# Optimization experiments

Hardware: AMD Instinct MI355X
Metric: run time of the kernel (lower is better)

The kernel has to match this reference:

```python
import jax, jax.numpy as jnp
import numpy as np

B, T, D_IN, P, Q, D_OUT = 128, 1024, 64, 128, 2, 64


def _lstm_layer(x, w_ih, w_hh, b):
    """One LSTM layer, batch_first. x: [B,T,Din], w_ih: [4P,Din], w_hh: [4P,P], b: [4P].
    PyTorch gate order: i, f, g, o."""
    # Precompute input contribution for all timesteps (the big, parallel GEMM).
    gx = jnp.einsum('btd,gd->btg', x, w_ih) + b          # [B,T,4P]
    gx_t = jnp.swapaxes(gx, 0, 1)                        # [T,B,4P] for scan
    p = w_hh.shape[1]
    h0 = jnp.zeros((x.shape[0], p), dtype=x.dtype)
    c0 = jnp.zeros((x.shape[0], p), dtype=x.dtype)

    def step(carry, g_in):
        h, c = carry
        g = g_in + h @ w_hh.T                            # [B,4P]
        i, f, gg, o = jnp.split(g, 4, axis=-1)
        i = jax.nn.sigmoid(i)
        f = jax.nn.sigmoid(f)
        gg = jnp.tanh(gg)
        o = jax.nn.sigmoid(o)
        c = f * c + i * gg
        h = o * jnp.tanh(c)
        return (h, c), h

    _, hs = jax.lax.scan(step, (h0, c0), gx_t)           # hs: [T,B,P]
    return jnp.swapaxes(hs, 0, 1)                        # [B,T,P]


def setup_inputs() -> dict:
    key = jax.random.key(0)
    ks = jax.random.split(key, 8)
    x = jax.random.normal(ks[0], (B, T, D_IN), dtype=jnp.float32)
    # weight_ih: kaiming-normal-ish; weight_hh: orthogonal-ish (random normal is a fine stand-in
    # numerically; init distribution doesn't change the math being tested).
    w_ih0 = jax.random.normal(ks[1], (4 * P, D_IN), dtype=jnp.float32) * (1.0 / np.sqrt(D_IN))
    w_hh0 = jax.random.normal(ks[2], (4 * P, P), dtype=jnp.float32) * (1.0 / np.sqrt(P))
    w_ih1 = jax.random.normal(ks[3], (4 * P, P), dtype=jnp.float32) * (1.0 / np.sqrt(P))
    w_hh1 = jax.random.normal(ks[4], (4 * P, P), dtype=jnp.float32) * (1.0 / np.sqrt(P))
    # biases initialized to zero in the original (bias_ih + bias_hh folded into one per layer
    # would be equivalent math; keep both for faithfulness)
    b_ih = jnp.zeros((Q, 4 * P), dtype=jnp.float32)
    b_hh = jnp.zeros((Q, 4 * P), dtype=jnp.float32)
    fc_w = jax.random.normal(ks[5], (D_OUT, P), dtype=jnp.float32) * np.sqrt(2.0 / P)
    fc_b = jnp.zeros((D_OUT,), dtype=jnp.float32)
    return {"x": x, "w_ih0": w_ih0, "w_hh0": w_hh0, "w_ih1": w_ih1, "w_hh1": w_hh1,
            "b_ih": b_ih, "b_hh": b_hh, "fc_w": fc_w, "fc_b": fc_b}


def reference(x, w_ih0, w_hh0, w_ih1, w_hh1, b_ih, b_hh, fc_w, fc_b):
    h = _lstm_layer(x, w_ih0, w_hh0, b_ih[0] + b_hh[0])   # layer 0: [B,T,P]
    h = _lstm_layer(h, w_ih1, w_hh1, b_ih[1] + b_hh[1])   # layer 1: [B,T,P]
    return jnp.einsum('btp,op->bto', h, fc_w) + fc_b      # [B,T,D_OUT]
```

## Files before the change

### kernel.cpp

```cpp
#include <hip/hip_runtime.h>

#define NT 1024
#define RINGS 256

typedef _Float16 half8 __attribute__((ext_vector_type(8)));
typedef _Float16 half4 __attribute__((ext_vector_type(4)));
typedef float f32x4 __attribute__((ext_vector_type(4)));
typedef unsigned long long u64;
struct U2 { u64 a, b; };

__device__ __forceinline__ f32x4 MFMA(half8 a, half8 b, f32x4 c) {
  return __builtin_amdgcn_mfma_f32_16x16x32_f16(a, b, c, 0, 0, 0);
}
__device__ __forceinline__ float sigf(float x) {
  return __builtin_amdgcn_rcpf(1.0f + __expf(-x));
}
__device__ __forceinline__ float tanhf2(float x) {
  float ax = fabsf(x);
  float e = __expf(-2.0f * ax);
  float t = (1.0f - e) * __builtin_amdgcn_rcpf(1.0f + e);
  return copysignf(t, x);
}
__device__ __forceinline__ half8 cvt8(float4 c0, float4 c1) {
  half8 hv;
  hv[0] = (_Float16)c0.x; hv[1] = (_Float16)c0.y;
  hv[2] = (_Float16)c0.z; hv[3] = (_Float16)c0.w;
  hv[4] = (_Float16)c1.x; hv[5] = (_Float16)c1.y;
  hv[6] = (_Float16)c1.z; hv[7] = (_Float16)c1.w;
  return hv;
}
__device__ __forceinline__ half8 ldring(const _Float16* p) {
  const u64* q = (const u64*)p;
  U2 uu;
  uu.a = __hip_atomic_load(q, __ATOMIC_RELAXED, __HIP_MEMORY_SCOPE_AGENT);
  uu.b = __hip_atomic_load(q + 1, __ATOMIC_RELAXED, __HIP_MEMORY_SCOPE_AGENT);
  return __builtin_bit_cast(half8, uu);
}
__device__ __forceinline__ unsigned wpoll(unsigned* p, unsigned tgt,
                                          unsigned cached, int l) {
  unsigned c = cached;
  while (c < tgt) {
    unsigned pv = 0;
    if (l == 0)
      pv = __hip_atomic_load(p, __ATOMIC_ACQUIRE, __HIP_MEMORY_SCOPE_AGENT);
    c = (unsigned)__builtin_amdgcn_readfirstlane((int)pv);
    if (c < tgt) __builtin_amdgcn_s_sleep(2);
  }
  return c;
}

__global__ __launch_bounds__(256) void prep_x(const float* __restrict__ x,
                                              _Float16* __restrict__ Xf) {
  int t0 = blockIdx.x * 256 + threadIdx.x;
  int l = t0 & 63;
  int fid = t0 >> 6;
  int kt = fid & 1;
  int t = (fid >> 1) & (NT - 1);
  int g = fid >> 11;
  int bt = g * 16 + (l & 15);
  int kb = kt * 32 + (l >> 4) * 4;
  const float* src = x + ((size_t)bt * NT + (size_t)t) * 64 + kb;
  float4 v0 = *(const float4*)src;
  float4 v1 = *(const float4*)(src + 16);
  *(half8*)(Xf + (size_t)fid * 512 + l * 8) = cvt8(v0, v1);
}

__global__ __launch_bounds__(512, 1) void lstm_main(
    const float* __restrict__ wih0, const float* __restrict__ whh0,
    const float* __restrict__ wih1, const float* __restrict__ whh1,
    const float* __restrict__ bih, const float* __restrict__ bhh,
    const float* __restrict__ fcw, const float* __restrict__ fcb,
    const _Float16* __restrict__ Xf, _Float16* __restrict__ ringH0,
    unsigned* __restrict__ flags, float* __restrict__ out) {
  const int tid = threadIdx.x;
  const int w = tid >> 6, l = tid & 63;
  const int n = l & 15, lg = l >> 4;
  const bool producer = blockIdx.x < 8;
  const int g = blockIdx.x & 7;

  __shared__ _Float16 hfr[2][4][64][8];
  __shared__ _Float16 fcl[4][4][64][8];

  _Float16* ringG = ringH0 + (size_t)g * RINGS * 2048;
  unsigned* prog = flags + g * 16;
  unsigned* cons = flags + (8 + g) * 16;
  const half8 hz = {0, 0, 0, 0, 0, 0, 0, 0};

  if (producer) {
    half8 A[4][6];
    f32x4 bias[4];
#pragma unroll
    for (int q = 0; q < 4; ++q) {
      int row = (w + 8 * q) * 16 + n;
#pragma unroll
      for (int kt = 0; kt < 2; ++kt) {
        const float* wp = wih0 + (size_t)row * 64 + kt * 32 + lg * 4;
        A[q][kt] = cvt8(*(const float4*)wp, *(const float4*)(wp + 16));
      }
#pragma unroll
      for (int kt = 0; kt < 4; ++kt) {
        const float* wp = whh0 + (size_t)row * 128 + kt * 32 + lg * 4;
        A[q][2 + kt] = cvt8(*(const float4*)wp, *(const float4*)(wp + 16));
      }
      int rb = (w + 8 * q) * 16 + lg * 4;
      f32x4 bv;
#pragma unroll
      for (int r = 0; r < 4; ++r) bv[r] = bih[rb + r] + bhh[rb + r];
      bias[q] = bv;
    }
    if (tid < 256) ((half8*)&hfr[1][0][0][0])[tid] = hz;
    const _Float16* XfG = Xf + (size_t)g * NT * 1024;
    half8 x0 = *(const half8*)(XfG + l * 8);
    half8 x1 = *(const half8*)(XfG + 512 + l * 8);
    f32x4 cst = {0.f, 0.f, 0.f, 0.f};
    unsigned Cc = 0;
    __syncthreads();
    for (int s = 0; s < NT; ++s) {
      half8 xn0, xn1;
      if (s + 1 < NT) {
        const _Float16* p = XfG + (size_t)(s + 1) * 1024 + l * 8;
        xn0 = *(const half8*)p;
        xn1 = *(const half8*)(p + 512);
      }
      if (s >= 224 && (s & 31) == 0)
        Cc = wpoll(cons, (unsigned)(s - 192), Cc, l);
      const int rdk = (s + 1) & 1;
      half8 b2 = *(const half8*)&hfr[rdk][0][l][0];
      half8 b3 = *(const half8*)&hfr[rdk][1][l][0];
      half8 b4 = *(const half8*)&hfr[rdk][2][l][0];
      half8 b5 = *(const half8*)&hfr[rdk][3][l][0];
      f32x4 acc0 = bias[0], acc1 = bias[1], acc2 = bias[2], acc3 = bias[3];
      acc0 = MFMA(A[0][0], x0, acc0); acc1 = MFMA(A[1][0], x0, acc1);
      acc2 = MFMA(A[2][0], x0, acc2); acc3 = MFMA(A[3][0], x0, acc3);
      acc0 = MFMA(A[0][1], x1, acc0); acc1 = MFMA(A[1][1], x1, acc1);
      acc2 = MFMA(A[2][1], x1, acc2); acc3 = MFMA(A[3][1], x1, acc3);
      acc0 = MFMA(A[0][2], b2, acc0); acc1 = MFMA(A[1][2], b2, acc1);
      acc2 = MFMA(A[2][2], b2, acc2); acc3 = MFMA(A[3][2], b2, acc3);
      acc0 = MFMA(A[0][3], b3, acc0); acc1 = MFMA(A[1][3], b3, acc1);
      acc2 = MFMA(A[2][3], b3, acc2); acc3 = MFMA(A[3][3], b3, acc3);
      acc0 = MFMA(A[0][4], b4, acc0); acc1 = MFMA(A[1][4], b4, acc1);
      acc2 = MFMA(A[2][4], b4, acc2); acc3 = MFMA(A[3][4], b4, acc3);
      acc0 = MFMA(A[0][5], b5, acc0); acc1 = MFMA(A[1][5], b5, acc1);
      acc2 = MFMA(A[2][5], b5, acc2); acc3 = MFMA(A[3][5], b5, acc3);
      half4 hh;
#pragma unroll
      for (int r = 0; r < 4; ++r) {
        float iv = sigf(acc0[r]), fv = sigf(acc1[r]);
        float gv = tanhf2(acc2[r]), ov = sigf(acc3[r]);
        cst[r] = fv * cst[r] + iv * gv;
        hh[r] = (_Float16)(ov * tanhf2(cst[r]));
      }
      *(half4*)&hfr[s & 1][w >> 1][l][(w & 1) << 2] = hh;
      {
        u64 uh = __builtin_bit_cast(u64, hh);
        __hip_atomic_store(
            (u64*)(ringG + (size_t)(s & (RINGS - 1)) * 2048 +
                   (w >> 1) * 512 + l * 8 + (w & 1) * 4),
            uh, __ATOMIC_RELAXED, __HIP_MEMORY_SCOPE_AGENT);
      }
      asm volatile("s_waitcnt lgkmcnt(0)" ::: "memory");
      __builtin_amdgcn_sched_barrier(0);
      __builtin_amdgcn_s_barrier();
      __builtin_amdgcn_sched_barrier(0);
      if ((s & 31) == 31) {
        asm volatile("s_waitcnt vmcnt(0)" ::: "memory");
        __builtin_amdgcn_sched_barrier(0);
        __builtin_amdgcn_s_barrier();
        __builtin_amdgcn_sched_barrier(0);
        if (tid == 0)
          __hip_atomic_store(prog, (unsigned)(s + 1), __ATOMIC_RELEASE,
                             __HIP_MEMORY_SCOPE_AGENT);
      }
      x0 = xn0;
      x1 = xn1;
    }
  } else {
    half8 A[4][8];
    f32x4 bias[4], fcbv = {0.f, 0.f, 0.f, 0.f};
#pragma unroll
    for (int q = 0; q < 4; ++q) {
      int row = (w + 8 * q) * 16 + n;
#pragma unroll
      for (int kt = 0; kt < 4; ++kt) {
        const float* wp = wih1 + (size_t)row * 128 + kt * 32 + lg * 4;
        A[q][kt] = cvt8(*(const float4*)wp, *(const float4*)(wp + 16));
      }
#pragma unroll
      for (int kt = 0; kt < 4; ++kt) {
        const float* wp = whh1 + (size_t)row * 128 + kt * 32 + lg * 4;
        A[q][4 + kt] = cvt8(*(const float4*)wp, *(const float4*)(wp + 16));
      }
      int rb = (w + 8 * q) * 16 + lg * 4;
      f32x4 bv;
#pragma unroll
      for (int r = 0; r < 4; ++r)
        bv[r] = bih[512 + rb + r] + bhh[512 + rb + r];
      bias[q] = bv;
    }
    if (w < 4) {
      int frow = (w << 4) + n;
#pragma unroll
      for (int kt = 0; kt < 4; ++kt) {
        const float* wp = fcw + (size_t)frow * 128 + kt * 32 + lg * 4;
        *(half8*)&fcl[w][kt][l][0] =
            cvt8(*(const float4*)wp, *(const float4*)(wp + 16));
      }
      fcbv = *(const f32x4*)(fcb + (w << 4) + lg * 4);
    }
    if (tid < 256) ((half8*)&hfr[1][0][0][0])[tid] = hz;
    float* outG = out + (size_t)((g << 4) + n) * NT * 64 + (w << 4) + lg * 4;
    f32x4 cst = {0.f, 0.f, 0.f, 0.f};
    __syncthreads();
    unsigned Pc = wpoll(prog, 2u, 0u, l);
    half8 hA0 = ldring(ringG + l * 8);
    half8 hA1 = ldring(ringG + 512 + l * 8);
    half8 hA2 = ldring(ringG + 1024 + l * 8);
    half8 hA3 = ldring(ringG + 1536 + l * 8);
    const _Float16* rb1 = ringG + 2048 + l * 8;
    half8 hB0 = ldring(rb1);
    half8 hB1 = ldring(rb1 + 512);
    half8 hB2 = ldring(rb1 + 1024);
    half8 hB3 = ldring(rb1 + 1536);

#define CSTEP(T, C0, C1, C2, C3)                                               \
  {                                                                            \
    const int rdk_ = ((T) + 1) & 1;                                            \
    half8 b4 = *(const half8*)&hfr[rdk_][0][l][0];                             \
    half8 b5 = *(const half8*)&hfr[rdk_][1][l][0];                             \
    half8 b6 = *(const half8*)&hfr[rdk_][2][l][0];                             \
    half8 b7 = *(const half8*)&hfr[rdk_][3][l][0];                             \
    f32x4 acc0 = bias[0], acc1 = bias[1], acc2 = bias[2], acc3 = bias[3];      \
    acc0 = MFMA(A[0][0], C0, acc0); acc1 = MFMA(A[1][0], C0, acc1);            \
    acc2 = MFMA(A[2][0], C0, acc2); acc3 = MFMA(A[3][0], C0, acc3);            \
    acc0 = MFMA(A[0][1], C1, acc0); acc1 = MFMA(A[1][1], C1, acc1);            \
    acc2 = MFMA(A[2][1], C1, acc2); acc3 = MFMA(A[3][1], C1, acc3);            \
    acc0 = MFMA(A[0][2], C2, acc0); acc1 = MFMA(A[1][2], C2, acc1);            \
    acc2 = MFMA(A[2][2], C2, acc2); acc3 = MFMA(A[3][2], C2, acc3);            \
    acc0 = MFMA(A[0][3], C3, acc0); acc1 = MFMA(A[1][3], C3, acc1);            \
    acc2 = MFMA(A[2][3], C3, acc2); acc3 = MFMA(A[3][3], C3, acc3);            \
    if ((T) + 2 < NT) {    \
      Pc = wpoll(prog, (unsigned)((T) + 3), Pc, l);                            \
      const _Float16* rb_ =                                                    \
          ringG + (size_t)(((T) + 2) & (RINGS - 1)) * 2048 + l * 8;            \
      C0 = ldring(rb_);        C1 = ldring(rb_ + 512);                         \
      C2 = ldring(rb_ + 1024); C3 = ldring(rb_ + 1536);                        \
    }                                                                          \
    acc0 = MFMA(A[0][4], b4, acc0); acc1 = MFMA(A[1][4], b4, acc1);            \
    acc2 = MFMA(A[2][4], b4, acc2); acc3 = MFMA(A[3][4], b4, acc3);            \
    acc0 = MFMA(A[0][5], b5, acc0); acc1 = MFMA(A[1][5], b5, acc1);            \
    acc2 = MFMA(A[2][5], b5, acc2); acc3 = MFMA(A[3][5], b5, acc3);            \
    acc0 = MFMA(A[0][6], b6, acc0); acc1 = MFMA(A[1][6], b6, acc1);            \
    acc2 = MFMA(A[2][6], b6, acc2); acc3 = MFMA(A[3][6], b6, acc3);            \
    acc0 = MFMA(A[0][7], b7, acc0); acc1 = MFMA(A[1][7], b7, acc1);            \
    acc2 = MFMA(A[2][7], b7, acc2); acc3 = MFMA(A[3][7], b7, acc3);            \
    if (w < 4) {                           \
      half8 f0 = *(const half8*)&fcl[w][0][l][0];                              \
      half8 f1 = *(const half8*)&fcl[w][1][l][0];                              \
      half8 f2 = *(const half8*)&fcl[w][2][l][0];                              \
      half8 f3 = *(const half8*)&fcl[w][3][l][0];                              \
      f32x4 afc = fcbv;                                                        \
      afc = MFMA(f0, b4, afc); afc = MFMA(f1, b5, afc);                        \
      afc = MFMA(f2, b6, afc); afc = MFMA(f3, b7, afc);                        \
      if ((T) >= 1) *(f32x4*)(outG + (size_t)((T) - 1) * 64) = afc;            \
    }                                                                          \
    half4 hh;                                                                  \
    _Pragma("unroll")                                                          \
    for (int r = 0; r < 4; ++r) {                                              \
      float iv = sigf(acc0[r]), fv = sigf(acc1[r]);                            \
      float gv = tanhf2(acc2[r]), ov = sigf(acc3[r]);                          \
      cst[r] = fv * cst[r] + iv * gv;                                          \
      hh[r] = (_Float16)(ov * tanhf2(cst[r]));                                 \
    }                                                                          \
    *(half4*)&hfr[(T) & 1][w >> 1][l][(w & 1) << 2] = hh;                      \
    if (tid == 0 && ((T) & 31) == 0)                                           \
      __hip_atomic_store(cons, (unsigned)(T), __ATOMIC_RELAXED,                \
                         __HIP_MEMORY_SCOPE_AGENT);                            \
    asm volatile("s_waitcnt lgkmcnt(0)" ::: "memory");                         \
    __builtin_amdgcn_sched_barrier(0);                                         \
    __builtin_amdgcn_s_barrier();        \
    __builtin_amdgcn_sched_barrier(0);                                         \
  }

    for (int t = 0; t < NT; t += 2) {
      CSTEP(t, hA0, hA1, hA2, hA3);
      CSTEP(t + 1, hB0, hB1, hB2, hB3);
    }
#undef CSTEP
    {
      half8 b4 = *(const half8*)&hfr[(NT + 1) & 1][0][l][0];
      half8 b5 = *(const half8*)&hfr[(NT + 1) & 1][1][l][0];
      half8 b6 = *(const half8*)&hfr[(NT + 1) & 1][2][l][0];
      half8 b7 = *(const half8*)&hfr[(NT + 1) & 1][3][l][0];
      if (w < 4) {
        half8 f0 = *(const half8*)&fcl[w][0][l][0];
        half8 f1 = *(const half8*)&fcl[w][1][l][0];
        half8 f2 = *(const half8*)&fcl[w][2][l][0];
        half8 f3 = *(const half8*)&fcl[w][3][l][0];
        f32x4 afc = fcbv;
        afc = MFMA(f0, b4, afc); afc = MFMA(f1, b5, afc);
        afc = MFMA(f2, b6, afc); afc = MFMA(f3, b7, afc);
        *(f32x4*)(outG + (size_t)(NT - 1) * 64) = afc;
      }
    }
  }
}

extern "C" void kernel_launch(void* const* d_in, const int* in_sizes, int n_in,
                              void* d_out, int out_size, void* d_ws, size_t ws_size,
                              hipStream_t stream) {
  const float* x     = (const float*)d_in[0];
  const float* w_ih0 = (const float*)d_in[1];
  const float* w_hh0 = (const float*)d_in[2];
  const float* w_ih1 = (const float*)d_in[3];
  const float* w_hh1 = (const float*)d_in[4];
  const float* b_ih  = (const float*)d_in[5];
  const float* b_hh  = (const float*)d_in[6];
  const float* fc_w  = (const float*)d_in[7];
  const float* fc_b  = (const float*)d_in[8];

  _Float16* Xf   = (_Float16*)d_ws;
  _Float16* ring = (_Float16*)((char*)d_ws + (16u << 20));
  unsigned* flags = (unsigned*)((char*)d_ws + (24u << 20));

  hipMemsetAsync(flags, 0, 4096, stream);
  prep_x<<<4096, 256, 0, stream>>>(x, Xf);
  lstm_main<<<16, 512, 0, stream>>>(w_ih0, w_hh0, w_ih1, w_hh1, b_ih, b_hh,
                                    fc_w, fc_b, Xf, ring, flags,
                                    (float*)d_out);
}
```

Measured before the change: 1.324 ms.

## Split fused producer/consumer LSTM kernel into two sequential layer kernels

Replaces the single kernel, where layer-0 blocks streamed hidden states through a ring buffer with flag polling to concurrently running layer-1 blocks, with two separate kernels run back to back. Layer 0 writes the full hidden sequence to workspace, then layer 1 reads it with plain loads. This removes the atomic ring traffic, the polling and the memset, but it serialises the two recurrences so the layers no longer overlap in time. The critical path roughly doubles, since both kernels are latency-bound over 1024 steps.

Measured after the change: 1.987 ms. 50.0% more time.

```diff
diff --git a/kernel.cpp b/kernel.cpp
--- a/kernel.cpp
+++ b/kernel.cpp
@@ -1,13 +1,11 @@
 #include <hip/hip_runtime.h>
 
 #define NT 1024
-#define RINGS 256
 
 typedef _Float16 half8 __attribute__((ext_vector_type(8)));
 typedef _Float16 half4 __attribute__((ext_vector_type(4)));
 typedef float f32x4 __attribute__((ext_vector_type(4)));
 typedef unsigned long long u64;
-struct U2 { u64 a, b; };
 
 __device__ __forceinline__ f32x4 MFMA(half8 a, half8 b, f32x4 c) {
   return __builtin_amdgcn_mfma_f32_16x16x32_f16(a, b, c, 0, 0, 0);
@@ -28,25 +26,6 @@
   hv[4] = (_Float16)c1.x; hv[5] = (_Float16)c1.y;
   hv[6] = (_Float16)c1.z; hv[7] = (_Float16)c1.w;
   return hv;
-}
-__device__ __forceinline__ half8 ldring(const _Float16* p) {
-  const u64* q = (const u64*)p;
-  U2 uu;
-  uu.a = __hip_atomic_load(q, __ATOMIC_RELAXED, __HIP_MEMORY_SCOPE_AGENT);
-  uu.b = __hip_atomic_load(q + 1, __ATOMIC_RELAXED, __HIP_MEMORY_SCOPE_AGENT);
-  return __builtin_bit_cast(half8, uu);
-}
-__device__ __forceinline__ unsigned wpoll(unsigned* p, unsigned tgt,
-                                          unsigned cached, int l) {
-  unsigned c = cached;
-  while (c < tgt) {
-    unsigned pv = 0;
-    if (l == 0)
-      pv = __hip_atomic_load(p, __ATOMIC_ACQUIRE, __HIP_MEMORY_SCOPE_AGENT);
-    c = (unsigned)__builtin_amdgcn_readfirstlane((int)pv);
-    if (c < tgt) __builtin_amdgcn_s_sleep(2);
-  }
-  return c;
 }
 
 __global__ __launch_bounds__(256) void prep_x(const float* __restrict__ x,
@@ -65,162 +44,151 @@
   *(half8*)(Xf + (size_t)fid * 512 + l * 8) = cvt8(v0, v1);
 }
 
-__global__ __launch_bounds__(512, 1) void lstm_main(
+__global__ __launch_bounds__(512, 1) void lstm_l0(
     const float* __restrict__ wih0, const float* __restrict__ whh0,
+    const float* __restrict__ bih, const float* __restrict__ bhh,
+    const _Float16* __restrict__ Xf, _Float16* __restrict__ h0f) {
+  const int tid = threadIdx.x;
+  const int w = tid >> 6, l = tid & 63;
+  const int n = l & 15, lg = l >> 4;
+  const int g = blockIdx.x;
+
+  __shared__ _Float16 hfr[2][4][64][8];
+  const half8 hz = {0, 0, 0, 0, 0, 0, 0, 0};
+
+  half8 A[4][6];
+  f32x4 bias[4];
+#pragma unroll
+  for (int q = 0; q < 4; ++q) {
+    int row = (w + 8 * q) * 16 + n;
+#pragma unroll
+    for (int kt = 0; kt < 2; ++kt) {
+      const float* wp = wih0 + (size_t)row * 64 + kt * 32 + lg * 4;
+      A[q][kt] = cvt8(*(const float4*)wp, *(const float4*)(wp + 16));
+    }
+#pragma unroll
+    for (int kt = 0; kt < 4; ++kt) {
+      const float* wp = whh0 + (size_t)row * 128 + kt * 32 + lg * 4;
+      A[q][2 + kt] = cvt8(*(const float4*)wp, *(const float4*)(wp + 16));
+    }
+    int rb = (w + 8 * q) * 16 + lg * 4;
+    f32x4 bv;
+#pragma unroll
+    for (int r = 0; r < 4; ++r) bv[r] = bih[rb + r] + bhh[rb + r];
+    bias[q] = bv;
+  }
+  if (tid < 256) ((half8*)&hfr[1][0][0][0])[tid] = hz;
+  const _Float16* XfG = Xf + (size_t)g * NT * 1024;
+  _Float16* h0G = h0f + (size_t)g * NT * 2048;
+  half8 x0 = *(const half8*)(XfG + l * 8);
+  half8 x1 = *(const half8*)(XfG + 512 + l * 8);
+  f32x4 cst = {0.f, 0.f, 0.f, 0.f};
+  __syncthreads();
+  for (int s = 0; s < NT; ++s) {
+    half8 xn0, xn1;
+    if (s + 1 < NT) {
+      const _Float16* p = XfG + (size_t)(s + 1) * 1024 + l * 8;
+      xn0 = *(const half8*)p;
+      xn1 = *(const half8*)(p + 512);
+    }
+    const int rdk = (s + 1) & 1;
+    half8 b2 = *(const half8*)&hfr[rdk][0][l][0];
+    half8 b3 = *(const half8*)&hfr[rdk][1][l][0];
+    half8 b4 = *(const half8*)&hfr[rdk][2][l][0];
+    half8 b5 = *(const half8*)&hfr[rdk][3][l][0];
+    f32x4 acc0 = bias[0], acc1 = bias[1], acc2 = bias[2], acc3 = bias[3];
+    acc0 = MFMA(A[0][0], x0, acc0); acc1 = MFMA(A[1][0], x0, acc1);
+    acc2 = MFMA(A[2][0], x0, acc2); acc3 = MFMA(A[3][0], x0, acc3);
+    acc0 = MFMA(A[0][1], x1, acc0); acc1 = MFMA(A[1][1], x1, acc1);
+    acc2 = MFMA(A[2][1], x1, acc2); acc3 = MFMA(A[3][1], x1, acc3);
+    acc0 = MFMA(A[0][2], b2, acc0); acc1 = MFMA(A[1][2], b2, acc1);
+    acc2 = MFMA(A[2][2], b2, acc2); acc3 = MFMA(A[3][2], b2, acc3);
+    acc0 = MFMA(A[0][3], b3, acc0); acc1 = MFMA(A[1][3], b3, acc1);
+    acc2 = MFMA(A[2][3], b3, acc2); acc3 = MFMA(A[3][3], b3, acc3);
+    acc0 = MFMA(A[0][4], b4, acc0); acc1 = MFMA(A[1][4], b4, acc1);
+    acc2 = MFMA(A[2][4], b4, acc2); acc3 = MFMA(A[3][4], b4, acc3);
+    acc0 = MFMA(A[0][5], b5, acc0); acc1 = MFMA(A[1][5], b5, acc1);
+    acc2 = MFMA(A[2][5], b5, acc2); acc3 = MFMA(A[3][5], b5, acc3);
+    half4 hh;
+#pragma unroll
+    for (int r = 0; r < 4; ++r) {
+      float iv = sigf(acc0[r]), fv = sigf(acc1[r]);
+      float gv = tanhf2(acc2[r]), ov = sigf(acc3[r]);
+      cst[r] = fv * cst[r] + iv * gv;
+      hh[r] = (_Float16)(ov * tanhf2(cst[r]));
+    }
+    *(half4*)&hfr[s & 1][w >> 1][l][(w & 1) << 2] = hh;
+    *(u64*)(h0G + (size_t)s * 2048 + (w >> 1) * 512 + l * 8 + (w & 1) * 4) =
+        __builtin_bit_cast(u64, hh);
+    asm volatile("s_waitcnt lgkmcnt(0)" ::: "memory");
+    __builtin_amdgcn_sched_barrier(0);
+    __builtin_amdgcn_s_barrier();
+    __builtin_amdgcn_sched_barrier(0);
+    x0 = xn0;
+    x1 = xn1;
+  }
+}
+
+__global__ __launch_bounds__(512, 1) void lstm_l1(
     const float* __restrict__ wih1, const float* __restrict__ whh1,
     const float* __restrict__ bih, const float* __restrict__ bhh,
     const float* __restrict__ fcw, const float* __restrict__ fcb,
-    const _Float16* __restrict__ Xf, _Float16* __restrict__ ringH0,
-    unsigned* __restrict__ flags, float* __restrict__ out) {
+    const _Float16* __restrict__ h0f, float* __restrict__ out) {
   const int tid = threadIdx.x;
   const int w = tid >> 6, l = tid & 63;
   const int n = l & 15, lg = l >> 4;
-  const bool producer = blockIdx.x < 8;
-  const int g = blockIdx.x & 7;
+  const int g = blockIdx.x;
 
   __shared__ _Float16 hfr[2][4][64][8];
   __shared__ _Float16 fcl[4][4][64][8];
-
-  _Float16* ringG = ringH0 + (size_t)g * RINGS * 2048;
-  unsigned* prog = flags + g * 16;
-  unsigned* cons = flags + (8 + g) * 16;
   const half8 hz = {0, 0, 0, 0, 0, 0, 0, 0};
 
-  if (producer) {
-    half8 A[4][6];
-    f32x4 bias[4];
-#pragma unroll
-    for (int q = 0; q < 4; ++q) {
-      int row = (w + 8 * q) * 16 + n;
-#pragma unroll
-      for (int kt = 0; kt < 2; ++kt) {
-        const float* wp = wih0 + (size_t)row * 64 + kt * 32 + lg * 4;
-        A[q][kt] = cvt8(*(const float4*)wp, *(const float4*)(wp + 16));
-      }
-#pragma unroll
-      for (int kt = 0; kt < 4; ++kt) {
-        const float* wp = whh0 + (size_t)row * 128 + kt * 32 + lg * 4;
-        A[q][2 + kt] = cvt8(*(const float4*)wp, *(const float4*)(wp + 16));
-      }
-      int rb = (w + 8 * q) * 16 + lg * 4;
-      f32x4 bv;
-#pragma unroll
-      for (int r = 0; r < 4; ++r) bv[r] = bih[rb + r] + bhh[rb + r];
-      bias[q] = bv;
-    }
-    if (tid < 256) ((half8*)&hfr[1][0][0][0])[tid] = hz;
-    const _Float16* XfG = Xf + (size_t)g * NT * 1024;
-    half8 x0 = *(const half8*)(XfG + l * 8);
-    half8 x1 = *(const half8*)(XfG + 512 + l * 8);
-    f32x4 cst = {0.f, 0.f, 0.f, 0.f};
-    unsigned Cc = 0;
-    __syncthreads();
-    for (int s = 0; s < NT; ++s) {
-      half8 xn0, xn1;
-      if (s + 1 < NT) {
-        const _Float16* p = XfG + (size_t)(s + 1) * 1024 + l * 8;
-        xn0 = *(const half8*)p;
-        xn1 = *(const half8*)(p + 512);
-      }
-      if (s >= 224 && (s & 31) == 0)
-        Cc = wpoll(cons, (unsigned)(s - 192), Cc, l);
-      const int rdk = (s + 1) & 1;
-      half8 b2 = *(const half8*)&hfr[rdk][0][l][0];
-      half8 b3 = *(const half8*)&hfr[rdk][1][l][0];
-      half8 b4 = *(const half8*)&hfr[rdk][2][l][0];
-      half8 b5 = *(const half8*)&hfr[rdk][3][l][0];
-      f32x4 acc0 = bias[0], acc1 = bias[1], acc2 = bias[2], acc3 = bias[3];
-      acc0 = MFMA(A[0][0], x0, acc0); acc1 = MFMA(A[1][0], x0, acc1);
-      acc2 = MFMA(A[2][0], x0, acc2); acc3 = MFMA(A[3][0], x0, acc3);
-      acc0 = MFMA(A[0][1], x1, acc0); acc1 = MFMA(A[1][1], x1, acc1);
-      acc2 = MFMA(A[2][1], x1, acc2); acc3 = MFMA(A[3][1], x1, acc3);
-      acc0 = MFMA(A[0][2], b2, acc0); acc1 = MFMA(A[1][2], b2, acc1);
-      acc2 = MFMA(A[2][2], b2, acc2); acc3 = MFMA(A[3][2], b2, acc3);
-      acc0 = MFMA(A[0][3], b3, acc0); acc1 = MFMA(A[1][3], b3, acc1);
-      acc2 = MFMA(A[2][3], b3, acc2); acc3 = MFMA(A[3][3], b3, acc3);
-      acc0 = MFMA(A[0][4], b4, acc0); acc1 = MFMA(A[1][4], b4, acc1);
-      acc2 = MFMA(A[2][4], b4, acc2); acc3 = MFMA(A[3][4], b4, acc3);
-      acc0 = MFMA(A[0][5], b5, acc0); acc1 = MFMA(A[1][5], b5, acc1);
-      acc2 = MFMA(A[2][5], b5, acc2); acc3 = MFMA(A[3][5], b5, acc3);
-      half4 hh;
-#pragma unroll
-      for (int r = 0; r < 4; ++r) {
-        float iv = sigf(acc0[r]), fv = sigf(acc1[r]);
-        float gv = tanhf2(acc2[r]), ov = sigf(acc3[r]);
-        cst[r] = fv * cst[r] + iv * gv;
-        hh[r] = (_Float16)(ov * tanhf2(cst[r]));
-      }
-      *(half4*)&hfr[s & 1][w >> 1][l][(w & 1) << 2] = hh;
-      {
-        u64 uh = __builtin_bit_cast(u64, hh);
-        __hip_atomic_store(
-            (u64*)(ringG + (size_t)(s & (RINGS - 1)) * 2048 +
-                   (w >> 1) * 512 + l * 8 + (w & 1) * 4),
-            uh, __ATOMIC_RELAXED, __HIP_MEMORY_SCOPE_AGENT);
-      }
-      asm volatile("s_waitcnt lgkmcnt(0)" ::: "memory");
-      __builtin_amdgcn_sched_barrier(0);
-      __builtin_amdgcn_s_barrier();
-      __builtin_amdgcn_sched_barrier(0);
-      if ((s & 31) == 31) {
-        asm volatile("s_waitcnt vmcnt(0)" ::: "memory");
-        __builtin_amdgcn_sched_barrier(0);
-        __builtin_amdgcn_s_barrier();
-        __builtin_amdgcn_sched_barrier(0);
-        if (tid == 0)
-          __hip_atomic_store(prog, (unsigned)(s + 1), __ATOMIC_RELEASE,
-                             __HIP_MEMORY_SCOPE_AGENT);
-      }
-      x0 = xn0;
-      x1 = xn1;
-    }
-  } else {
-    half8 A[4][8];
-    f32x4 bias[4], fcbv = {0.f, 0.f, 0.f, 0.f};
-#pragma unroll
-    for (int q = 0; q < 4; ++q) {
-      int row = (w + 8 * q) * 16 + n;
-#pragma unroll
-      for (int kt = 0; kt < 4; ++kt) {
-        const float* wp = wih1 + (size_t)row * 128 + kt * 32 + lg * 4;
-        A[q][kt] = cvt8(*(const float4*)wp, *(const float4*)(wp + 16));
-      }
-#pragma unroll
-      for (int kt = 0; kt < 4; ++kt) {
-        const float* wp = whh1 + (size_t)row * 128 + kt * 32 + lg * 4;
-        A[q][4 + kt] = cvt8(*(const float4*)wp, *(const float4*)(wp + 16));
-      }
-      int rb = (w + 8 * q) * 16 + lg * 4;
-      f32x4 bv;
-#pragma unroll
-      for (int r = 0; r < 4; ++r)
-        bv[r] = bih[512 + rb + r] + bhh[512 + rb + r];
-      bias[q] = bv;
-    }
-    if (w < 4) {
-      int frow = (w << 4) + n;
-#pragma unroll
-      for (int kt = 0; kt < 4; ++kt) {
-        const float* wp = fcw + (size_t)frow * 128 + kt * 32 + lg * 4;
-        *(half8*)&fcl[w][kt][l][0] =
-            cvt8(*(const float4*)wp, *(const float4*)(wp + 16));
-      }
-      fcbv = *(const f32x4*)(fcb + (w << 4) + lg * 4);
-    }
-    if (tid < 256) ((half8*)&hfr[1][0][0][0])[tid] = hz;
-    float* outG = out + (size_t)((g << 4) + n) * NT * 64 + (w << 4) + lg * 4;
-    f32x4 cst = {0.f, 0.f, 0.f, 0.f};
-    __syncthreads();
-    unsigned Pc = wpoll(prog, 2u, 0u, l);
-    half8 hA0 = ldring(ringG + l * 8);
-    half8 hA1 = ldring(ringG + 512 + l * 8);
-    half8 hA2 = ldring(ringG + 1024 + l * 8);
-    half8 hA3 = ldring(ringG + 1536 + l * 8);
-    const _Float16* rb1 = ringG + 2048 + l * 8;
-    half8 hB0 = ldring(rb1);
-    half8 hB1 = ldring(rb1 + 512);
-    half8 hB2 = ldring(rb1 + 1024);
-    half8 hB3 = ldring(rb1 + 1536);
+  half8 A[4][8];
+  f32x4 bias[4], fcbv = {0.f, 0.f, 0.f, 0.f};
+#pragma unroll
+  for (int q = 0; q < 4; ++q) {
+    int row = (w + 8 * q) * 16 + n;
+#pragma unroll
+    for (int kt = 0; kt < 4; ++kt) {
+      const float* wp = wih1 + (size_t)row * 128 + kt * 32 + lg * 4;
+      A[q][kt] = cvt8(*(const float4*)wp, *(const float4*)(wp + 16));
+    }
+#pragma unroll
+    for (int kt = 0; kt < 4; ++kt) {
+      const float* wp = whh1 + (size_t)row * 128 + kt * 32 + lg * 4;
+      A[q][4 + kt] = cvt8(*(const float4*)wp, *(const float4*)(wp + 16));
+    }
+    int rb = (w + 8 * q) * 16 + lg * 4;
+    f32x4 bv;
+#pragma unroll
+    for (int r = 0; r < 4; ++r)
+      bv[r] = bih[512 + rb + r] + bhh[512 + rb + r];
+    bias[q] = bv;
+  }
+  if (w < 4) {
+    int frow = (w << 4) + n;
+#pragma unroll
+    for (int kt = 0; kt < 4; ++kt) {
+      const float* wp = fcw + (size_t)frow * 128 + kt * 32 + lg * 4;
+      *(half8*)&fcl[w][kt][l][0] =
+          cvt8(*(const float4*)wp, *(const float4*)(wp + 16));
+    }
+    fcbv = *(const f32x4*)(fcb + (w << 4) + lg * 4);
+  }
+  if (tid < 256) ((half8*)&hfr[1][0][0][0])[tid] = hz;
+  const _Float16* h0G = h0f + (size_t)g * NT * 2048;
+  float* outG = out + (size_t)((g << 4) + n) * NT * 64 + (w << 4) + lg * 4;
+  f32x4 cst = {0.f, 0.f, 0.f, 0.f};
+  __syncthreads();
+  half8 hA0 = *(const half8*)(h0G + l * 8);
+  half8 hA1 = *(const half8*)(h0G + 512 + l * 8);
+  half8 hA2 = *(const half8*)(h0G + 1024 + l * 8);
+  half8 hA3 = *(const half8*)(h0G + 1536 + l * 8);
+  const _Float16* h1p = h0G + 2048 + l * 8;
+  half8 hB0 = *(const half8*)(h1p);
+  half8 hB1 = *(const half8*)(h1p + 512);
+  half8 hB2 = *(const half8*)(h1p + 1024);
+  half8 hB3 = *(const half8*)(h1p + 1536);
 
 #define CSTEP(T, C0, C1, C2, C3)                                               \
   {                                                                            \
@@ -238,12 +206,12 @@
     acc2 = MFMA(A[2][2], C2, acc2); acc3 = MFMA(A[3][2], C2, acc3);            \
     acc0 = MFMA(A[0][3], C3, acc0); acc1 = MFMA(A[1][3], C3, acc1);            \
     acc2 = MFMA(A[2][3], C3, acc2); acc3 = MFMA(A[3][3], C3, acc3);            \
-    if ((T) + 2 < NT) {    \
-      Pc = wpoll(prog, (unsigned)((T) + 3), Pc, l);                            \
-      const _Float16* rb_ =                                                    \
-          ringG + (size_t)(((T) + 2) & (RINGS - 1)) * 2048 + l * 8;            \
-      C0 = ldring(rb_);        C1 = ldring(rb_ + 512);                         \
-      C2 = ldring(rb_ + 1024); C3 = ldring(rb_ + 1536);                        \
+    if ((T) + 2 < NT) {   \
+      const _Float16* hp_ = h0G + (size_t)((T) + 2) * 2048 + l * 8;            \
+      C0 = *(const half8*)(hp_);                                               \
+      C1 = *(const half8*)(hp_ + 512);                                         \
+      C2 = *(const half8*)(hp_ + 1024);                                        \
+      C3 = *(const half8*)(hp_ + 1536);                                        \
     }                                                                          \
     acc0 = MFMA(A[0][4], b4, acc0); acc1 = MFMA(A[1][4], b4, acc1);            \
     acc2 = MFMA(A[2][4], b4, acc2); acc3 = MFMA(A[3][4], b4, acc3);            \
@@ -272,35 +240,31 @@
       hh[r] = (_Float16)(ov * tanhf2(cst[r]));                                 \
     }                                                                          \
     *(half4*)&hfr[(T) & 1][w >> 1][l][(w & 1) << 2] = hh;                      \
-    if (tid == 0 && ((T) & 31) == 0)                                           \
-      __hip_atomic_store(cons, (unsigned)(T), __ATOMIC_RELAXED,                \
-                         __HIP_MEMORY_SCOPE_AGENT);                            \
     asm volatile("s_waitcnt lgkmcnt(0)" ::: "memory");                         \
     __builtin_amdgcn_sched_barrier(0);                                         \
-    __builtin_amdgcn_s_barrier();        \
+    __builtin_amdgcn_s_barrier();             \
     __builtin_amdgcn_sched_barrier(0);                                         \
   }
 
-    for (int t = 0; t < NT; t += 2) {
-      CSTEP(t, hA0, hA1, hA2, hA3);
-      CSTEP(t + 1, hB0, hB1, hB2, hB3);
-    }
+  for (int t = 0; t < NT; t += 2) {
+    CSTEP(t, hA0, hA1, hA2, hA3);
+    CSTEP(t + 1, hB0, hB1, hB2, hB3);
+  }
 #undef CSTEP
-    {
-      half8 b4 = *(const half8*)&hfr[(NT + 1) & 1][0][l][0];
-      half8 b5 = *(const half8*)&hfr[(NT + 1) & 1][1][l][0];
-      half8 b6 = *(const half8*)&hfr[(NT + 1) & 1][2][l][0];
-      half8 b7 = *(const half8*)&hfr[(NT + 1) & 1][3][l][0];
-      if (w < 4) {
-        half8 f0 = *(const half8*)&fcl[w][0][l][0];
-        half8 f1 = *(const half8*)&fcl[w][1][l][0];
-        half8 f2 = *(const half8*)&fcl[w][2][l][0];
-        half8 f3 = *(const half8*)&fcl[w][3][l][0];
-        f32x4 afc = fcbv;
-        afc = MFMA(f0, b4, afc); afc = MFMA(f1, b5, afc);
-        afc = MFMA(f2, b6, afc); afc = MFMA(f3, b7, afc);
-        *(f32x4*)(outG + (size_t)(NT - 1) * 64) = afc;
-      }
+  {
+    half8 b4 = *(const half8*)&hfr[(NT + 1) & 1][0][l][0];
+    half8 b5 = *(const half8*)&hfr[(NT + 1) & 1][1][l][0];
+    half8 b6 = *(const half8*)&hfr[(NT + 1) & 1][2][l][0];
+    half8 b7 = *(const half8*)&hfr[(NT + 1) & 1][3][l][0];
+    if (w < 4) {
+      half8 f0 = *(const half8*)&fcl[w][0][l][0];
+      half8 f1 = *(const half8*)&fcl[w][1][l][0];
+      half8 f2 = *(const half8*)&fcl[w][2][l][0];
+      half8 f3 = *(const half8*)&fcl[w][3][l][0];
+      f32x4 afc = fcbv;
+      afc = MFMA(f0, b4, afc); afc = MFMA(f1, b5, afc);
+      afc = MFMA(f2, b6, afc); afc = MFMA(f3, b7, afc);
+      *(f32x4*)(outG + (size_t)(NT - 1) * 64) = afc;
     }
   }
 }
@@ -318,13 +282,11 @@
   const float* fc_w  = (const float*)d_in[7];
   const float* fc_b  = (const float*)d_in[8];
 
-  _Float16* Xf   = (_Float16*)d_ws;
-  _Float16* ring = (_Float16*)((char*)d_ws + (16u << 20));
-  unsigned* flags = (unsigned*)((char*)d_ws + (24u << 20));
-
-  hipMemsetAsync(flags, 0, 4096, stream);
+  _Float16* Xf  = (_Float16*)d_ws;
+  _Float16* h0f = (_Float16*)((char*)d_ws + (16u << 20));
+
   prep_x<<<4096, 256, 0, stream>>>(x, Xf);
-  lstm_main<<<16, 512, 0, stream>>>(w_ih0, w_hh0, w_ih1, w_hh1, b_ih, b_hh,
-                                    fc_w, fc_b, Xf, ring, flags,
-                                    (float*)d_out);
-}
+  lstm_l0<<<8, 512, 0, stream>>>(w_ih0, w_hh0, b_ih, b_hh, Xf, h0f);
+  lstm_l1<<<8, 512, 0, stream>>>(w_ih1, w_hh1, b_ih, b_hh, fc_w, fc_b, h0f,
+                                 (float*)d_out);
+}
```
